# Optimization experiments

Measured on AMD Instinct MI355X. Metric: run time of the kernel, lower is better.

The kernel has to match this reference:

```python
import jax, jax.numpy as jnp
import numpy as np

B, S, K, V = 512, 1024, 128, 512
SCALE = float(np.sqrt(K))


def setup_inputs() -> dict:
    key0 = jax.random.key(0)
    ks = jax.random.split(key0, 16)
    inp = {
        "keys": jax.random.normal(ks[0], (B, S, K), jnp.float32),
        "values": jax.random.normal(ks[1], (B, S, V), jnp.float32),
        "key": jax.random.normal(ks[2], (B, K), jnp.float32),
        "value": jax.random.normal(ks[3], (B, V), jnp.float32),
        "hidden": jax.random.normal(ks[4], (B, V), jnp.float32),
        "write_ptr": jax.random.randint(ks[5], (B,), 0, S, jnp.int64).astype(jnp.int64),
        "filled": jax.random.randint(ks[6], (B,), 0, S, jnp.int64).astype(jnp.int64),
        # parameters (Linear: y = x @ W.T + b)
        "Wq": jax.random.normal(ks[7], (K, V), jnp.float32) / np.sqrt(V),
        "bq": jnp.zeros((K,), jnp.float32),
        "Wg1": jax.random.normal(ks[8], (V, 2 * V), jnp.float32) / np.sqrt(2 * V),
        "bg1": jnp.zeros((V,), jnp.float32),
        "Wg2": jax.random.normal(ks[9], (V, V), jnp.float32) / np.sqrt(V),
        "bg2": jnp.zeros((V,), jnp.float32),
        "Wo": jax.random.normal(ks[10], (V, V), jnp.float32) / np.sqrt(V),
        "bo": jnp.zeros((V,), jnp.float32),
    }
    return inp


def reference(keys, values, key, value, hidden, write_ptr, filled,
              Wq, bq, Wg1, bg1, Wg2, bg2, Wo, bo):
    b_idx = jnp.arange(B)
    # --- write (ring-buffer scatter; torch does it under no_grad) ---
    keys_w = keys.at[b_idx, write_ptr].set(jax.lax.stop_gradient(key))
    values_w = values.at[b_idx, write_ptr].set(jax.lax.stop_gradient(value))
    filled_w = jnp.minimum(filled + 1, S)
    # --- read ---
    query = hidden @ Wq.T + bq                                  # (B, K)
    scores = jnp.einsum('bsk,bk->bs', keys_w, query) / SCALE     # (B, S)
    valid = jnp.arange(S)[None, :] < filled_w[:, None]           # (B, S)
    scores = jnp.where(valid, scores, -jnp.inf)
    attn = jax.nn.softmax(scores, axis=-1)
    attn = jnp.nan_to_num(attn, nan=0.0)
    retrieved = jnp.einsum('bs,bsv->bv', attn, values_w)         # (B, V)
    h_cat = jnp.concatenate([hidden, retrieved], axis=-1)        # (B, 2V)
    g = jax.nn.silu(h_cat @ Wg1.T + bg1)
    gate = jax.nn.sigmoid(g @ Wg2.T + bg2)
    out = (hidden + gate * retrieved) @ Wo.T + bo                # (B, V)
    return out
```

## Files before the change

### kernel.cpp

```cpp
#include <hip/hip_runtime.h>
#include <math.h>

#define BB 512
#define SS 1024
#define KK 128
#define VV 512
#define NC 16
#define CH 64
#define KS 8
#define QB 8

static constexpr float INV_SCALE = 0.088388347648318447f;

typedef float nfloat4 __attribute__((ext_vector_type(4)));

__device__ __forceinline__ float4 ntload(const float4* p) {
    nfloat4 v = __builtin_nontemporal_load((const nfloat4*)p);
    return make_float4(v.x, v.y, v.z, v.w);
}

__global__ __launch_bounds__(256) void q_kernel(
    const float* __restrict__ hidden, const float* __restrict__ Wq,
    const float* __restrict__ bq, float* __restrict__ qout)
{
    __shared__ float hidb[QB][516];
    __shared__ float wqt[16][516];
    __shared__ float qp[16][QB][2];
    const int blk = blockIdx.x;
    const int t = threadIdx.x;
    const int b0 = blk * QB;

    for (int i = t; i < QB * 128; i += 256) {
        const int bl = i >> 7, c4 = i & 127;
        *(float4*)&hidb[bl][c4 * 4] =
            ((const float4*)(hidden + (size_t)(b0 + bl) * VV))[c4];
    }
    for (int k0 = 0; k0 < KK; k0 += 16) {
        __syncthreads();
        for (int i = t; i < 16 * 128; i += 256) {
            const int kl = i >> 7, c4 = i & 127;
            *(float4*)&wqt[kl][c4 * 4] =
                ((const float4*)(Wq + (size_t)(k0 + kl) * VV))[c4];
        }
        __syncthreads();
        {
            const int p = t & 127, half = t >> 7;
            const int kl = p >> 3, bl = p & 7;
            const float* wr = &wqt[kl][half * 256];
            const float* hr = &hidb[bl][half * 256];
            float acc = 0.f;
            #pragma unroll
            for (int j = 0; j < 64; ++j) {
                const float4 wv = *(const float4*)&wr[j * 4];
                const float4 hv = *(const float4*)&hr[j * 4];
                acc += wv.x * hv.x + wv.y * hv.y + wv.z * hv.z + wv.w * hv.w;
            }
            qp[kl][bl][half] = acc;
        }
        __syncthreads();
        if (t < 128) {
            const int kl = t >> 3, bl = t & 7;
            qout[(size_t)(b0 + bl) * KK + k0 + kl] =
                qp[kl][bl][0] + qp[kl][bl][1] + bq[k0 + kl];
        }
    }
}

__global__ __launch_bounds__(256) void attn_chunk_kernel(
    const float* __restrict__ keys, const float* __restrict__ values,
    const float* __restrict__ keyv, const float* __restrict__ valv,
    const float* __restrict__ q,
    const int* __restrict__ write_ptr, const int* __restrict__ filled,
    float* __restrict__ ml, float* __restrict__ accp)
{
    __shared__ __align__(16) float qs[KK];
    __shared__ __align__(16) float p[CH];
    __shared__ __align__(16) float red[4];
    __shared__ __align__(16) float4 pvp[VV / 4];

    const int bc = blockIdx.x;
    const int b = bc >> 4;
    const int c = bc & 15;
    const int t = threadIdx.x;
    const int wave = t >> 6, lane = t & 63;

    int f = filled[b] + 1; if (f > SS) f = SS;
    const int sbeg = c * CH;
    int n = f - sbeg; if (n > CH) n = CH;

    float* mlrow = ml + ((size_t)b * NC + c) * 2;
    float* arow  = accp + ((size_t)b * NC + c) * VV;

    if (n <= 0) {
        if (t == 0) { mlrow[0] = -INFINITY; mlrow[1] = 0.f; }
        return;
    }

    if (t < KK / 4) ((float4*)qs)[t] = ((const float4*)(q + (size_t)b * KK))[t];
    __syncthreads();

    const int sub = lane & 31, rsel = lane >> 5;
    const int srow = wave * 2 + rsel;
    const float4 q4 = ((const float4*)qs)[sub];
    const float* kb = keys + ((size_t)b * SS + sbeg) * KK;
    const float* kw = keyv + (size_t)b * KK;
    const int wpl = write_ptr[b] - sbeg;

    const int nmain = n & ~31;
    for (int s0 = 0; s0 < nmain; s0 += 32) {
        float4 kv[4];
        #pragma unroll
        for (int u = 0; u < 4; ++u) {
            const int s = s0 + u * 8 + srow;
            const float* kr = (s == wpl) ? kw : (kb + (size_t)s * KK);
            kv[u] = ntload(((const float4*)kr) + sub);
        }
        #pragma unroll
        for (int u = 0; u < 4; ++u) {
            float prt = kv[u].x * q4.x + kv[u].y * q4.y
                      + kv[u].z * q4.z + kv[u].w * q4.w;
            prt += __shfl_xor(prt, 16);
            prt += __shfl_xor(prt, 8);
            prt += __shfl_xor(prt, 4);
            prt += __shfl_xor(prt, 2);
            prt += __shfl_xor(prt, 1);
            if (sub == 0) p[s0 + u * 8 + srow] = prt * INV_SCALE;
        }
    }
    for (int s = nmain + srow; s < n; s += 8) {
        const float* kr = (s == wpl) ? kw : (kb + (size_t)s * KK);
        const float4 kv = ntload(((const float4*)kr) + sub);
        float prt = kv.x * q4.x + kv.y * q4.y + kv.z * q4.z + kv.w * q4.w;
        prt += __shfl_xor(prt, 16);
        prt += __shfl_xor(prt, 8);
        prt += __shfl_xor(prt, 4);
        prt += __shfl_xor(prt, 2);
        prt += __shfl_xor(prt, 1);
        if (sub == 0) p[s] = prt * INV_SCALE;
    }
    __syncthreads();

    float lmax = -INFINITY;
    for (int i = t; i < n; i += 256) lmax = fmaxf(lmax, p[i]);
    lmax = fmaxf(lmax, __shfl_xor(lmax, 32));
    lmax = fmaxf(lmax, __shfl_xor(lmax, 16));
    lmax = fmaxf(lmax, __shfl_xor(lmax, 8));
    lmax = fmaxf(lmax, __shfl_xor(lmax, 4));
    lmax = fmaxf(lmax, __shfl_xor(lmax, 2));
    lmax = fmaxf(lmax, __shfl_xor(lmax, 1));
    if (lane == 0) red[wave] = lmax;
    __syncthreads();
    const float m = fmaxf(fmaxf(red[0], red[1]), fmaxf(red[2], red[3]));
    float lsum = 0.f;
    for (int i = t; i < n; i += 256) {
        const float e = __expf(p[i] - m);
        p[i] = e;
        lsum += e;
    }
    lsum += __shfl_xor(lsum, 32);
    lsum += __shfl_xor(lsum, 16);
    lsum += __shfl_xor(lsum, 8);
    lsum += __shfl_xor(lsum, 4);
    lsum += __shfl_xor(lsum, 2);
    lsum += __shfl_xor(lsum, 1);
    __syncthreads();
    if (lane == 0) red[wave] = lsum;
    __syncthreads();
    const float l = red[0] + red[1] + red[2] + red[3];

    const int col4 = t & 127, stream = t >> 7;
    const float4* vb = (const float4*)(values + ((size_t)b * SS + sbeg) * VV);
    const float4* vw = (const float4*)(valv + (size_t)b * VV);
    float4 acc = make_float4(0.f, 0.f, 0.f, 0.f);
    const int nm2 = n & ~15;
    for (int s0 = 0; s0 < nm2; s0 += 16) {
        float4 v[8]; float ps[8];
        #pragma unroll
        for (int u = 0; u < 8; ++u) {
            const int s = s0 + u * 2 + stream;
            const float4* vr = (s == wpl) ? vw : (vb + (size_t)s * (VV / 4));
            v[u] = ntload(vr + col4);
            ps[u] = p[s];
        }
        #pragma unroll
        for (int u = 0; u < 8; ++u) {
            acc.x += ps[u] * v[u].x;
            acc.y += ps[u] * v[u].y;
            acc.z += ps[u] * v[u].z;
            acc.w += ps[u] * v[u].w;
        }
    }
    for (int s = nm2 + stream; s < n; s += 2) {
        const float4* vr = (s == wpl) ? vw : (vb + (size_t)s * (VV / 4));
        const float4 v = ntload(vr + col4);
        const float psv = p[s];
        acc.x += psv * v.x;
        acc.y += psv * v.y;
        acc.z += psv * v.z;
        acc.w += psv * v.w;
    }
    if (stream == 1) pvp[col4] = acc;
    __syncthreads();
    if (stream == 0) {
        const float4 o = pvp[col4];
        ((float4*)arow)[col4] = make_float4(acc.x + o.x, acc.y + o.y,
                                            acc.z + o.z, acc.w + o.w);
    }
    if (t == 0) { mlrow[0] = m; mlrow[1] = l; }
}

__global__ __launch_bounds__(128) void combine_kernel(
    const float* __restrict__ hidden, const float* __restrict__ ml,
    const float* __restrict__ accp, float* __restrict__ hcat)
{
    const int b = blockIdx.x, t = threadIdx.x;
    const float* mlb = ml + (size_t)b * NC * 2;
    float mv[NC], lv[NC];
    #pragma unroll
    for (int c = 0; c < NC; ++c) { mv[c] = mlb[2 * c]; lv[c] = mlb[2 * c + 1]; }
    float ms = mv[0];
    #pragma unroll
    for (int c = 1; c < NC; ++c) ms = fmaxf(ms, mv[c]);
    float w[NC], denom = 0.f;
    #pragma unroll
    for (int c = 0; c < NC; ++c) { w[c] = __expf(mv[c] - ms); denom += w[c] * lv[c]; }
    const float invd = 1.f / denom;
    float4 r = make_float4(0.f, 0.f, 0.f, 0.f);
    for (int c = 0; c < NC; ++c) {
        if (lv[c] != 0.f) {
            const float4 x = ((const float4*)(accp + ((size_t)b * NC + c) * VV))[t];
            r.x += w[c] * x.x; r.y += w[c] * x.y;
            r.z += w[c] * x.z; r.w += w[c] * x.w;
        }
    }
    r.x *= invd; r.y *= invd; r.z *= invd; r.w *= invd;
    float4* hc = (float4*)(hcat + (size_t)b * 2 * VV);
    hc[t] = ((const float4*)(hidden + (size_t)b * VV))[t];
    hc[VV / 4 + t] = r;
}

__global__ __launch_bounds__(256) void gemm_ks_kernel(
    const float* __restrict__ Agl, int K, const float* __restrict__ W,
    const float* __restrict__ prev, const float* __restrict__ bias,
    const float* __restrict__ hc, float* __restrict__ part, int mode)
{
    __shared__ __align__(16) float As[2][16][68];
    __shared__ __align__(16) float Bs[2][16][68];
    const int bx = blockIdx.x;
    const int mt = bx & 7, nt = (bx >> 3) & 7, ks = bx >> 6;
    const int kseg = K >> 3;
    const int kbeg = ks * kseg, kend = kbeg + kseg;
    const int t = threadIdx.x;
    const int tx = t & 15, ty = t >> 4;
    const int m0 = mt << 6, n0 = nt << 6;
    const int ra = t >> 2, ca = (t & 3) << 2;
    const size_t pst = (size_t)VV * VV;
    float4 a0 = {0,0,0,0}, a1 = {0,0,0,0}, a2 = {0,0,0,0}, a3 = {0,0,0,0};

    auto loadA = [&](int k0) -> float4 {
        if (mode == 0)
            return *(const float4*)(Agl + (size_t)(m0 + ra) * K + k0 + ca);
        const size_t off = (size_t)(m0 + ra) * VV + k0 + ca;
        float4 s = *(const float4*)(bias + k0 + ca);
        #pragma unroll
        for (int sx = 0; sx < KS; ++sx) {
            const float4 pv = *(const float4*)(prev + (size_t)sx * pst + off);
            s.x += pv.x; s.y += pv.y; s.z += pv.z; s.w += pv.w;
        }
        float4 av;
        if (mode == 1) {
            av.x = s.x / (1.f + __expf(-s.x));
            av.y = s.y / (1.f + __expf(-s.y));
            av.z = s.z / (1.f + __expf(-s.z));
            av.w = s.w / (1.f + __expf(-s.w));
        } else {
            const float4 h  = *(const float4*)(hc + (size_t)(m0 + ra) * (2 * VV) + k0 + ca);
            const float4 rr = *(const float4*)(hc + (size_t)(m0 + ra) * (2 * VV) + VV + k0 + ca);
            av.x = h.x + rr.x / (1.f + __expf(-s.x));
            av.y = h.y + rr.y / (1.f + __expf(-s.y));
            av.z = h.z + rr.z / (1.f + __expf(-s.z));
            av.w = h.w + rr.w / (1.f + __expf(-s.w));
        }
        return av;
    };

    {
        const float4 av = loadA(kbeg);
        const float4 wv = *(const float4*)(W + (size_t)(n0 + ra) * K + kbeg + ca);
        As[0][ca + 0][ra] = av.x; As[0][ca + 1][ra] = av.y;
        As[0][ca + 2][ra] = av.z; As[0][ca + 3][ra] = av.w;
        Bs[0][ca + 0][ra] = wv.x; Bs[0][ca + 1][ra] = wv.y;
        Bs[0][ca + 2][ra] = wv.z; Bs[0][ca + 3][ra] = wv.w;
    }
    __syncthreads();

    int cur = 0;
    for (int k0 = kbeg; k0 < kend; k0 += 16) {
        const int knext = k0 + 16;
        const bool has = (knext < kend);
        float4 av2, wv2;
        if (has) {
            av2 = loadA(knext);
            wv2 = *(const float4*)(W + (size_t)(n0 + ra) * K + knext + ca);
        }
        #pragma unroll
        for (int k = 0; k < 16; ++k) {
            const float4 a = *(const float4*)&As[cur][k][ty << 2];
            const float4 b = *(const float4*)&Bs[cur][k][tx << 2];
            a0.x += a.x * b.x; a0.y += a.x * b.y; a0.z += a.x * b.z; a0.w += a.x * b.w;
            a1.x += a.y * b.x; a1.y += a.y * b.y; a1.z += a.y * b.z; a1.w += a.y * b.w;
            a2.x += a.z * b.x; a2.y += a.z * b.y; a2.z += a.z * b.z; a2.w += a.z * b.w;
            a3.x += a.w * b.x; a3.y += a.w * b.y; a3.z += a.w * b.z; a3.w += a.w * b.w;
        }
        if (has) {
            const int nb = cur ^ 1;
            As[nb][ca + 0][ra] = av2.x; As[nb][ca + 1][ra] = av2.y;
            As[nb][ca + 2][ra] = av2.z; As[nb][ca + 3][ra] = av2.w;
            Bs[nb][ca + 0][ra] = wv2.x; Bs[nb][ca + 1][ra] = wv2.y;
            Bs[nb][ca + 2][ra] = wv2.z; Bs[nb][ca + 3][ra] = wv2.w;
        }
        __syncthreads();
        cur ^= 1;
    }

    float* pp = part + (size_t)ks * pst
              + (size_t)(m0 + (ty << 2)) * VV + n0 + (tx << 2);
    *(float4*)(pp + 0 * VV) = a0;
    *(float4*)(pp + 1 * VV) = a1;
    *(float4*)(pp + 2 * VV) = a2;
    *(float4*)(pp + 3 * VV) = a3;
}

__global__ __launch_bounds__(128) void reduce_bias_kernel(
    const float* __restrict__ part, const float* __restrict__ bo,
    float* __restrict__ out)
{
    const int b = blockIdx.x, t = threadIdx.x;
    const size_t o = (size_t)b * (VV / 4) + t;
    const size_t st = (size_t)VV * (VV / 4);
    const float4* p4 = (const float4*)part;
    const float4 bb = ((const float4*)bo)[t];
    float4 s = bb;
    #pragma unroll
    for (int k = 0; k < KS; ++k) {
        const float4 pv = p4[o + (size_t)k * st];
        s.x += pv.x; s.y += pv.y; s.z += pv.z; s.w += pv.w;
    }
    ((float4*)out)[o] = s;
}

extern "C" void kernel_launch(void* const* d_in, const int* in_sizes, int n_in,
                              void* d_out, int out_size, void* d_ws, size_t ws_size,
                              hipStream_t stream) {
    const float* keys    = (const float*)d_in[0];
    const float* values  = (const float*)d_in[1];
    const float* keyv    = (const float*)d_in[2];
    const float* valv    = (const float*)d_in[3];
    const float* hidden  = (const float*)d_in[4];
    const int*   wptr    = (const int*)d_in[5];
    const int*   filled  = (const int*)d_in[6];
    const float* Wq  = (const float*)d_in[7];
    const float* bq  = (const float*)d_in[8];
    const float* Wg1 = (const float*)d_in[9];
    const float* bg1 = (const float*)d_in[10];
    const float* Wg2 = (const float*)d_in[11];
    const float* bg2 = (const float*)d_in[12];
    const float* Wo  = (const float*)d_in[13];
    const float* bo  = (const float*)d_in[14];
    float* out = (float*)d_out;

    float* ws    = (float*)d_ws;
    float* q     = ws;
    float* ml    = q + (size_t)BB * KK;
    float* accp  = ml + (size_t)BB * NC * 2;
    float* hcat  = accp + (size_t)BB * NC * VV;
    float* part1 = hcat + (size_t)BB * 2 * VV;
    float* part2 = part1 + (size_t)KS * VV * VV;
    float* part3 = part2 + (size_t)KS * VV * VV;

    q_kernel<<<BB / QB, 256, 0, stream>>>(hidden, Wq, bq, q);
    attn_chunk_kernel<<<BB * NC, 256, 0, stream>>>(keys, values, keyv, valv, q,
                                                   wptr, filled, ml, accp);
    combine_kernel<<<BB, 128, 0, stream>>>(hidden, ml, accp, hcat);

    gemm_ks_kernel<<<64 * KS, 256, 0, stream>>>(hcat, 2 * VV, Wg1,
                                                nullptr, nullptr, nullptr,
                                                part1, 0);
    gemm_ks_kernel<<<64 * KS, 256, 0, stream>>>(nullptr, VV, Wg2,
                                                part1, bg1, nullptr,
                                                part2, 1);
    gemm_ks_kernel<<<64 * KS, 256, 0, stream>>>(nullptr, VV, Wo,
                                                part2, bg2, hcat,
                                                part3, 2);
    reduce_bias_kernel<<<BB, 128, 0, stream>>>(part3, bo, out);
}
```

Baseline: 203.7 us.

## Halve attention chunk count and replace final split-K reduce with atomics

The attention stage now uses 8 chunks of 128 positions per batch row instead of 16 chunks of 64, which halves the partial accumulators written and combined. The final output GEMM no longer writes split-K partials for a separate reduce kernel. It atomically adds into the output, which the combine kernel pre-initializes with the bias. This removes one kernel launch and a round trip of partial buffers, at the cost of float atomics contention and non-deterministic summation order.

```diff
diff --git a/kernel.cpp b/kernel.cpp
--- a/kernel.cpp
+++ b/kernel.cpp
@@ -5,8 +5,8 @@
 #define SS 1024
 #define KK 128
 #define VV 512
-#define NC 16
-#define CH 64
+#define NC 8
+#define CH 128
 #define KS 8
 #define QB 8
 
@@ -79,8 +79,8 @@
     __shared__ __align__(16) float4 pvp[VV / 4];
 
     const int bc = blockIdx.x;
-    const int b = bc >> 4;
-    const int c = bc & 15;
+    const int b = bc >> 3;
+    const int c = bc & 7;
     const int t = threadIdx.x;
     const int wave = t >> 6, lane = t & 63;
 
@@ -211,7 +211,8 @@
 
 __global__ __launch_bounds__(128) void combine_kernel(
     const float* __restrict__ hidden, const float* __restrict__ ml,
-    const float* __restrict__ accp, float* __restrict__ hcat)
+    const float* __restrict__ accp, float* __restrict__ hcat,
+    const float* __restrict__ bo, float* __restrict__ out)
 {
     const int b = blockIdx.x, t = threadIdx.x;
     const float* mlb = ml + (size_t)b * NC * 2;
@@ -237,12 +238,13 @@
     float4* hc = (float4*)(hcat + (size_t)b * 2 * VV);
     hc[t] = ((const float4*)(hidden + (size_t)b * VV))[t];
     hc[VV / 4 + t] = r;
+    ((float4*)(out + (size_t)b * VV))[t] = ((const float4*)bo)[t];
 }
 
 __global__ __launch_bounds__(256) void gemm_ks_kernel(
     const float* __restrict__ Agl, int K, const float* __restrict__ W,
     const float* __restrict__ prev, const float* __restrict__ bias,
-    const float* __restrict__ hc, float* __restrict__ part, int mode)
+    const float* __restrict__ hc, float* __restrict__ dst, int mode)
 {
     __shared__ __align__(16) float As[2][16][68];
     __shared__ __align__(16) float Bs[2][16][68];
@@ -323,30 +325,24 @@
         cur ^= 1;
     }
 
-    float* pp = part + (size_t)ks * pst
-              + (size_t)(m0 + (ty << 2)) * VV + n0 + (tx << 2);
-    *(float4*)(pp + 0 * VV) = a0;
-    *(float4*)(pp + 1 * VV) = a1;
-    *(float4*)(pp + 2 * VV) = a2;
-    *(float4*)(pp + 3 * VV) = a3;
-}
-
-__global__ __launch_bounds__(128) void reduce_bias_kernel(
-    const float* __restrict__ part, const float* __restrict__ bo,
-    float* __restrict__ out)
-{
-    const int b = blockIdx.x, t = threadIdx.x;
-    const size_t o = (size_t)b * (VV / 4) + t;
-    const size_t st = (size_t)VV * (VV / 4);
-    const float4* p4 = (const float4*)part;
-    const float4 bb = ((const float4*)bo)[t];
-    float4 s = bb;
-    #pragma unroll
-    for (int k = 0; k < KS; ++k) {
-        const float4 pv = p4[o + (size_t)k * st];
-        s.x += pv.x; s.y += pv.y; s.z += pv.z; s.w += pv.w;
-    }
-    ((float4*)out)[o] = s;
+    if (mode == 2) {
+        float* op = dst + (size_t)(m0 + (ty << 2)) * VV + n0 + (tx << 2);
+        const float4 rws[4] = {a0, a1, a2, a3};
+        #pragma unroll
+        for (int r = 0; r < 4; ++r) {
+            atomicAdd(op + r * VV + 0, rws[r].x);
+            atomicAdd(op + r * VV + 1, rws[r].y);
+            atomicAdd(op + r * VV + 2, rws[r].z);
+            atomicAdd(op + r * VV + 3, rws[r].w);
+        }
+    } else {
+        float* pp = dst + (size_t)ks * pst
+                  + (size_t)(m0 + (ty << 2)) * VV + n0 + (tx << 2);
+        *(float4*)(pp + 0 * VV) = a0;
+        *(float4*)(pp + 1 * VV) = a1;
+        *(float4*)(pp + 2 * VV) = a2;
+        *(float4*)(pp + 3 * VV) = a3;
+    }
 }
 
 extern "C" void kernel_launch(void* const* d_in, const int* in_sizes, int n_in,
@@ -376,12 +372,11 @@
     float* hcat  = accp + (size_t)BB * NC * VV;
     float* part1 = hcat + (size_t)BB * 2 * VV;
     float* part2 = part1 + (size_t)KS * VV * VV;
-    float* part3 = part2 + (size_t)KS * VV * VV;
 
     q_kernel<<<BB / QB, 256, 0, stream>>>(hidden, Wq, bq, q);
     attn_chunk_kernel<<<BB * NC, 256, 0, stream>>>(keys, values, keyv, valv, q,
                                                    wptr, filled, ml, accp);
-    combine_kernel<<<BB, 128, 0, stream>>>(hidden, ml, accp, hcat);
+    combine_kernel<<<BB, 128, 0, stream>>>(hidden, ml, accp, hcat, bo, out);
 
     gemm_ks_kernel<<<64 * KS, 256, 0, stream>>>(hcat, 2 * VV, Wg1,
                                                 nullptr, nullptr, nullptr,
@@ -391,6 +386,5 @@
                                                 part2, 1);
     gemm_ks_kernel<<<64 * KS, 256, 0, stream>>>(nullptr, VV, Wo,
                                                 part2, bg2, hcat,
-                                                part3, 2);
-    reduce_bias_kernel<<<BB, 128, 0, stream>>>(part3, bo, out);
-}
+                                                out, 2);
+}
```

After: 250.6 us. 23.0% more time.
